# Optimization experiments

Measured on AMD Instinct MI355X. Metric: run time of the kernel, lower is better.

Reference implementation:

```python
import jax, jax.numpy as jnp
import numpy as np

N_NODES = 100000
N_EDGES = 800000
D_IN = 128
HOPS = 2
BN_EPS = 1e-5


def setup_inputs() -> dict:
    key = jax.random.key(0)
    ks = jax.random.split(key, 12)
    d_cat = D_IN * (HOPS + 1)  # 384
    inp = {
        "x": jax.random.normal(ks[0], (N_NODES, D_IN), dtype=jnp.float32),
        "edge_index": jax.random.randint(ks[1], (2, N_EDGES), 0, N_NODES, dtype=jnp.int32),
        "W0": jax.random.normal(ks[2], (HOPS + 1, D_IN, D_IN), dtype=jnp.float32) / np.sqrt(D_IN),
        "b0": jax.random.normal(ks[3], (HOPS + 1, D_IN), dtype=jnp.float32) * 0.01,
        "W1": jax.random.normal(ks[4], (HOPS + 1, d_cat, D_IN), dtype=jnp.float32) / np.sqrt(d_cat),
        "b1": jax.random.normal(ks[5], (HOPS + 1, D_IN), dtype=jnp.float32) * 0.01,
        "W2": jax.random.normal(ks[6], (HOPS + 1, d_cat, D_IN), dtype=jnp.float32) / np.sqrt(d_cat),
        "b2": jax.random.normal(ks[7], (HOPS + 1, D_IN), dtype=jnp.float32) * 0.01,
        "bn_gamma": jnp.ones((2, d_cat), dtype=jnp.float32),
        "bn_beta": jnp.zeros((2, d_cat), dtype=jnp.float32),
    }
    return inp


def _gcn_norm(edge_index, n):
    # gcn_norm(add_self_loops=False): deg over col, w_e = d^-1/2[row]*d^-1/2[col]
    row, col = edge_index[0], edge_index[1]
    deg = jax.ops.segment_sum(jnp.ones(row.shape[0], jnp.float32), col, num_segments=n)
    dinv = jnp.where(deg > 0, jax.lax.rsqrt(jnp.maximum(deg, 1.0)), 0.0)
    w = dinv[row] * dinv[col]
    return row, col, w


def _spmm(row, col, w, xj, n):
    # adj_t = SparseTensor(row=col, col=row, value=w): out[col_e] += w_e * x[row_e]
    return jax.ops.segment_sum(w[:, None] * xj[row], col, num_segments=n)


def _mixhop_layer(x, W, b, row, col, w, n):
    outs = [x @ W[0] + b[0]]
    for j in range(1, HOPS + 1):
        xj = x @ W[j] + b[j]
        for _ in range(j):
            xj = _spmm(row, col, w, xj, n)
        outs.append(xj)
    return jnp.concatenate(outs, axis=1)


def _bn(x, g, b):
    mu = jnp.mean(x, axis=0)
    var = jnp.mean(jnp.square(x - mu), axis=0)
    return (x - mu) * jax.lax.rsqrt(var + BN_EPS) * g + b


def reference(x, edge_index, W0, b0, W1, b1, W2, b2, bn_gamma, bn_beta):
    n = x.shape[0]
    row, col, w = _gcn_norm(edge_index, n)
    h = _mixhop_layer(x, W0, b0, row, col, w, n)
    h = jax.nn.relu(_bn(h, bn_gamma[0], bn_beta[0]))  # dropout: eval mode (identity)
    h = _mixhop_layer(h, W1, b1, row, col, w, n)
    h = jax.nn.relu(_bn(h, bn_gamma[1], bn_beta[1]))
    h = _mixhop_layer(h, W2, b2, row, col, w, n)
    return h
```

## Files before the change

### kernel.cpp

```cpp
#include <hip/hip_runtime.h>
#include <hip/hip_bf16.h>

#define NN 100000
#define NE 800000
#define DIN 128
#define DCAT 384
#define BN_EPS 1e-5

typedef __attribute__((ext_vector_type(8))) short bf16x8;
typedef __attribute__((ext_vector_type(4))) float f32x4;


__global__ void count_deg_k(const int* __restrict__ ei, int* __restrict__ deg) {
    int i = blockIdx.x * blockDim.x + threadIdx.x;
    if (i < NE) atomicAdd(&deg[ei[NE + i]], 1);
}

__global__ void dinv_k(const int* __restrict__ deg, float* __restrict__ dinv) {
    int i = blockIdx.x * blockDim.x + threadIdx.x;
    if (i < NN) {
        int d = deg[i];
        dinv[i] = (d > 0) ? rsqrtf((float)d) : 0.f;
    }
}

__global__ void scan1_k(const int* __restrict__ deg, int* __restrict__ out,
                        int* __restrict__ bsum) {
    __shared__ int s[1024];
    int i = blockIdx.x * 1024 + threadIdx.x;
    int v = (i < NN) ? deg[i] : 0;
    s[threadIdx.x] = v;
    __syncthreads();
    for (int off = 1; off < 1024; off <<= 1) {
        int t = (threadIdx.x >= off) ? s[threadIdx.x - off] : 0;
        __syncthreads();
        s[threadIdx.x] += t;
        __syncthreads();
    }
    if (i < NN) out[i] = s[threadIdx.x] - v;
    if (threadIdx.x == 1023) bsum[blockIdx.x] = s[1023];
}

__global__ void scan2_k(int* __restrict__ bsum, int nb) {
    if (threadIdx.x == 0) {
        int acc = 0;
        for (int b = 0; b < nb; ++b) { int v = bsum[b]; bsum[b] = acc; acc += v; }
    }
}

__global__ void scan3_k(int* __restrict__ ptr, int* __restrict__ cursor,
                        const int* __restrict__ bsum) {
    int i = blockIdx.x * 1024 + threadIdx.x;
    if (i < NN) {
        int p = ptr[i] + bsum[blockIdx.x];
        ptr[i] = p;
        cursor[i] = p;
    }
    if (i == NN) ptr[NN] = NE;
}

__global__ void scatter_k(const int* __restrict__ ei, const float* __restrict__ dinv,
                          int* __restrict__ cursor, int* __restrict__ crow,
                          float* __restrict__ cw) {
    int i = blockIdx.x * blockDim.x + threadIdx.x;
    if (i >= NE) return;
    int r = ei[i];
    int c = ei[NE + i];
    int p = atomicAdd(&cursor[c], 1);
    crow[p] = r;
    cw[p] = dinv[r] * dinv[c];
}


__device__ inline void split_trunc(float x, short& hi, short& lo) {
    unsigned u = __builtin_bit_cast(unsigned, x);
    hi = (short)(u >> 16);
    float hf = __builtin_bit_cast(float, u & 0xFFFF0000u);
    __hip_bfloat16 l = __float2bfloat16(x - hf);
    lo = *reinterpret_cast<short*>(&l);
}

__global__ void wsplit_k(const float* __restrict__ W, int K,
                         short* __restrict__ Wth, short* __restrict__ Wtl) {
    int i = blockIdx.x * 256 + threadIdx.x;
    if (i >= 3 * K * 128) return;
    int c = i & 127;
    int k = (i >> 7) % K;
    int j = i / (K * 128);
    short h, l;
    split_trunc(W[i], h, l);
    size_t o = (size_t)j * 128 * 384 + (size_t)c * 384 + k;
    Wth[o] = h;
    Wtl[o] = l;
}

#define GPITCH 40

__global__ __launch_bounds__(256, 2) void gemm3m_k(
    const float* __restrict__ X, int K,
    const short* __restrict__ Wth, const short* __restrict__ Wtl,
    const float* __restrict__ bias,
    const float2* __restrict__ coef, int use_bn,
    float* __restrict__ o0, float* __restrict__ o1, float* __restrict__ o2) {
    __shared__ short As_h[128 * GPITCH];
    __shared__ short As_l[128 * GPITCH];
    __shared__ short Bs_h[128 * GPITCH];
    __shared__ short Bs_l[128 * GPITCH];

    const int nwg = gridDim.x;
    const int id  = blockIdx.x;
    const int q = nwg >> 3, r = nwg & 7;
    const int xcd = id & 7, ii = id >> 3;
    const int swz = (xcd < r ? xcd * (q + 1) : r * (q + 1) + (xcd - r) * q) + ii;
    const int j  = swz % 3;
    const int my = swz / 3;
    const int m0 = my * 128;

    const int t    = threadIdx.x;
    const int lane = t & 63;
    const int wv   = t >> 6;
    const int wr   = (wv >> 1) * 64;
    const int wc   = (wv & 1) * 64;
    const int lr   = lane & 15;
    const int lk   = lane >> 4;

    const short* Wh = Wth + (size_t)j * 128 * 384;
    const short* Wl = Wtl + (size_t)j * 128 * 384;

    f32x4 acc[4][4];
#pragma unroll
    for (int a = 0; a < 4; ++a)
#pragma unroll
        for (int b = 0; b < 4; ++b) acc[a][b] = (f32x4){0.f, 0.f, 0.f, 0.f};

    for (int kb = 0; kb < K; kb += 32) {
#pragma unroll
        for (int i = 0; i < 4; ++i) {
            int lin = t + i * 256;
            int row = lin >> 3, kq = lin & 7;
            int gr = m0 + row;
            if (gr >= NN) gr = NN - 1;
            float4 a4 = *(const float4*)(X + (size_t)gr * K + kb + kq * 4);
            if (use_bn) {
                int c = kb + kq * 4;
                float2 c0 = coef[c + 0], c1 = coef[c + 1], c2 = coef[c + 2], c3 = coef[c + 3];
                a4.x = fmaxf(a4.x * c0.x + c0.y, 0.f);
                a4.y = fmaxf(a4.y * c1.x + c1.y, 0.f);
                a4.z = fmaxf(a4.z * c2.x + c2.y, 0.f);
                a4.w = fmaxf(a4.w * c3.x + c3.y, 0.f);
            }
            short h0, l0, h1, l1, h2, l2, h3, l3;
            split_trunc(a4.x, h0, l0);
            split_trunc(a4.y, h1, l1);
            split_trunc(a4.z, h2, l2);
            split_trunc(a4.w, h3, l3);
            *(short4*)&As_h[row * GPITCH + kq * 4] = make_short4(h0, h1, h2, h3);
            *(short4*)&As_l[row * GPITCH + kq * 4] = make_short4(l0, l1, l2, l3);
        }
#pragma unroll
        for (int i = 0; i < 4; ++i) {
            int lin = t + i * 256;
            int col = lin >> 3, kq = lin & 7;
            short4 bh = *(const short4*)(Wh + (size_t)col * 384 + kb + kq * 4);
            short4 bl = *(const short4*)(Wl + (size_t)col * 384 + kb + kq * 4);
            *(short4*)&Bs_h[col * GPITCH + kq * 4] = bh;
            *(short4*)&Bs_l[col * GPITCH + kq * 4] = bl;
        }
        __syncthreads();

        bf16x8 ah[4], al[4];
#pragma unroll
        for (int mr = 0; mr < 4; ++mr) {
            int rr = wr + mr * 16 + lr;
            ah[mr] = *(const bf16x8*)&As_h[rr * GPITCH + lk * 8];
            al[mr] = *(const bf16x8*)&As_l[rr * GPITCH + lk * 8];
        }
#pragma unroll
        for (int nc = 0; nc < 4; ++nc) {
            int c = wc + nc * 16 + lr;
            bf16x8 bh = *(const bf16x8*)&Bs_h[c * GPITCH + lk * 8];
            bf16x8 bl = *(const bf16x8*)&Bs_l[c * GPITCH + lk * 8];
#pragma unroll
            for (int mr = 0; mr < 4; ++mr) {
                f32x4 a = acc[mr][nc];
                a = __builtin_amdgcn_mfma_f32_16x16x32_bf16(al[mr], bh, a, 0, 0, 0);
                a = __builtin_amdgcn_mfma_f32_16x16x32_bf16(ah[mr], bl, a, 0, 0, 0);
                a = __builtin_amdgcn_mfma_f32_16x16x32_bf16(ah[mr], bh, a, 0, 0, 0);
                acc[mr][nc] = a;
            }
        }
        __syncthreads();
    }

    float* dst;
    int pitch;
    if (j == 0)      { dst = o0; pitch = DCAT; }
    else if (j == 1) { dst = o1; pitch = 128; }
    else             { dst = o2; pitch = 128; }

#pragma unroll
    for (int nc = 0; nc < 4; ++nc) {
        int col = wc + nc * 16 + lr;
        float bv = bias[j * 128 + col];
#pragma unroll
        for (int mr = 0; mr < 4; ++mr) {
            f32x4 a = acc[mr][nc];
#pragma unroll
            for (int rr = 0; rr < 4; ++rr) {
                int row = m0 + wr + mr * 16 + lk * 4 + rr;
                if (row < NN) dst[(size_t)row * pitch + col] = a[rr] + bv;
            }
        }
    }
}

__global__ __launch_bounds__(256) void spmm2_k(
    const int* __restrict__ ptr, const int* __restrict__ rows,
    const float* __restrict__ wv,
    const float* __restrict__ inA, const float* __restrict__ inB,
    float* __restrict__ outA, int poutA,
    float* __restrict__ outB) {
    int wid  = (blockIdx.x * blockDim.x + threadIdx.x) >> 6;
    int lane = threadIdx.x & 63;
    if (wid >= NN) return;
    int e0 = ptr[wid], e1 = ptr[wid + 1];
    float2 aA = make_float2(0.f, 0.f), aB = make_float2(0.f, 0.f);
    int e = e0;
    for (; e + 2 <= e1; e += 2) {
        int   r0 = rows[e],  r1 = rows[e + 1];
        float w0 = wv[e],    w1 = wv[e + 1];
        float2 vA0 = ((const float2*)(inA + (size_t)r0 * 128))[lane];
        float2 vB0 = ((const float2*)(inB + (size_t)r0 * 128))[lane];
        float2 vA1 = ((const float2*)(inA + (size_t)r1 * 128))[lane];
        float2 vB1 = ((const float2*)(inB + (size_t)r1 * 128))[lane];
        aA.x += w0 * vA0.x; aA.y += w0 * vA0.y;
        aB.x += w0 * vB0.x; aB.y += w0 * vB0.y;
        aA.x += w1 * vA1.x; aA.y += w1 * vA1.y;
        aB.x += w1 * vB1.x; aB.y += w1 * vB1.y;
    }
    if (e < e1) {
        int   r0 = rows[e];
        float w0 = wv[e];
        float2 vA0 = ((const float2*)(inA + (size_t)r0 * 128))[lane];
        float2 vB0 = ((const float2*)(inB + (size_t)r0 * 128))[lane];
        aA.x += w0 * vA0.x; aA.y += w0 * vA0.y;
        aB.x += w0 * vB0.x; aB.y += w0 * vB0.y;
    }
    ((float2*)(outA + (size_t)wid * poutA))[lane] = aA;
    ((float2*)(outB + (size_t)wid * 128))[lane] = aB;
}

__global__ __launch_bounds__(256) void spmm_k(
    const int* __restrict__ ptr, const int* __restrict__ rows,
    const float* __restrict__ wv, const float* __restrict__ xin, int pin,
    float* __restrict__ xout, int pout) {
    int wid  = (blockIdx.x * blockDim.x + threadIdx.x) >> 6;
    int lane = threadIdx.x & 63;
    if (wid >= NN) return;
    int e0 = ptr[wid], e1 = ptr[wid + 1];
    float2 acc = make_float2(0.f, 0.f);
    int e = e0;
    for (; e + 4 <= e1; e += 4) {
        int   r0 = rows[e],     r1 = rows[e + 1], r2 = rows[e + 2], r3 = rows[e + 3];
        float w0 = wv[e],       w1 = wv[e + 1],   w2 = wv[e + 2],   w3 = wv[e + 3];
        float2 v0 = ((const float2*)(xin + (size_t)r0 * pin))[lane];
        float2 v1 = ((const float2*)(xin + (size_t)r1 * pin))[lane];
        float2 v2 = ((const float2*)(xin + (size_t)r2 * pin))[lane];
        float2 v3 = ((const float2*)(xin + (size_t)r3 * pin))[lane];
        acc.x += w0 * v0.x; acc.y += w0 * v0.y;
        acc.x += w1 * v1.x; acc.y += w1 * v1.y;
        acc.x += w2 * v2.x; acc.y += w2 * v2.y;
        acc.x += w3 * v3.x; acc.y += w3 * v3.y;
    }
    for (; e < e1; ++e) {
        int   r0 = rows[e];
        float w0 = wv[e];
        float2 v0 = ((const float2*)(xin + (size_t)r0 * pin))[lane];
        acc.x += w0 * v0.x; acc.y += w0 * v0.y;
    }
    ((float2*)(xout + (size_t)wid * pout))[lane] = acc;
}

#define BN_ROWS 256
#define BN_NBLK ((NN + BN_ROWS - 1) / BN_ROWS)

__global__ void bn_stats1_k(const float* __restrict__ H, float* __restrict__ partial) {
    int c  = threadIdx.x;
    int r0 = blockIdx.x * BN_ROWS;
    int r1 = min(r0 + BN_ROWS, NN);
    float s = 0.f, s2 = 0.f;
    for (int r = r0; r < r1; ++r) {
        float v = H[(size_t)r * DCAT + c];
        s  += v;
        s2 += v * v;
    }
    partial[blockIdx.x * 768 + c]       = s;
    partial[blockIdx.x * 768 + 384 + c] = s2;
}

__global__ void bn_finalize_k(const float* __restrict__ partial,
                              const float* __restrict__ g, const float* __restrict__ b,
                              float2* __restrict__ coef) {
    int c = threadIdx.x;
    double s = 0.0, s2 = 0.0;
    for (int i = 0; i < BN_NBLK; ++i) {
        s  += (double)partial[i * 768 + c];
        s2 += (double)partial[i * 768 + 384 + c];
    }
    double mu  = s / (double)NN;
    double var = s2 / (double)NN - mu * mu;
    double inv = 1.0 / sqrt(var + (double)BN_EPS);
    float scale = (float)((double)g[c] * inv);
    float shift = (float)((double)b[c] - mu * (double)g[c] * inv);
    coef[c] = make_float2(scale, shift);
}


static void run_layer(const float* X, int K, const float* W, const float* bias,
                      const float2* coefIn, int use_bn,
                      float* Hout, float* tmpA, float* tmpB, float* tmpC,
                      short* Wth, short* Wtl,
                      const int* ptr, const int* crow, const float* cw,
                      hipStream_t stream) {
    int nw = 3 * K * 128;
    wsplit_k<<<(nw + 255) / 256, 256, 0, stream>>>(W, K, Wth, Wtl);
    int nwg = 3 * ((NN + 127) / 128);
    gemm3m_k<<<nwg, 256, 0, stream>>>(X, K, Wth, Wtl, bias, coefIn, use_bn,
                                      Hout, tmpA, tmpB);
    int sg = (NN * 64 + 255) / 256;
    spmm2_k<<<sg, 256, 0, stream>>>(ptr, crow, cw, tmpA, tmpB, Hout + 128, DCAT, tmpC);
    spmm_k<<<sg, 256, 0, stream>>>(ptr, crow, cw, tmpC, 128, Hout + 256, DCAT);
}

static void run_bn_stats(const float* H, const float* g, const float* b,
                         float* partial, float2* coef, hipStream_t stream) {
    bn_stats1_k<<<BN_NBLK, 384, 0, stream>>>(H, partial);
    bn_finalize_k<<<1, 384, 0, stream>>>(partial, g, b, coef);
}

extern "C" void kernel_launch(void* const* d_in, const int* in_sizes, int n_in,
                              void* d_out, int out_size, void* d_ws, size_t ws_size,
                              hipStream_t stream) {
    const float* x        = (const float*)d_in[0];
    const int*   ei       = (const int*)d_in[1];
    const float* W0       = (const float*)d_in[2];
    const float* b0       = (const float*)d_in[3];
    const float* W1       = (const float*)d_in[4];
    const float* b1       = (const float*)d_in[5];
    const float* W2       = (const float*)d_in[6];
    const float* b2       = (const float*)d_in[7];
    const float* bn_gamma = (const float*)d_in[8];
    const float* bn_beta  = (const float*)d_in[9];
    float* out = (float*)d_out;

    char* p = (char*)d_ws;
    auto alloc = [&](size_t bytes) -> void* {
        void* r = (void*)p;
        p += (bytes + 511) & ~(size_t)511;
        return r;
    };
    float* Hws     = (float*)alloc((size_t)NN * DCAT * 4);
    float* tmpA    = (float*)alloc((size_t)NN * 128 * 4);
    float* tmpB    = (float*)alloc((size_t)NN * 128 * 4);
    int*   deg     = (int*)alloc((size_t)NN * 4);
    float* dinv    = (float*)alloc((size_t)NN * 4);
    int*   ptr     = (int*)alloc((size_t)(NN + 1) * 4);
    int*   cursor  = (int*)alloc((size_t)NN * 4);
    int*   bsum    = (int*)alloc(1024);
    int*   crow    = (int*)alloc((size_t)NE * 4);
    float* cw      = (float*)alloc((size_t)NE * 4);
    float* partial = (float*)alloc((size_t)BN_NBLK * 768 * 4);
    float2* coef   = (float2*)alloc(384 * 8);
    short* Wth     = (short*)alloc((size_t)3 * 128 * 384 * 2);
    short* Wtl     = (short*)alloc((size_t)3 * 128 * 384 * 2);

    hipMemsetAsync(deg, 0, (size_t)NN * 4, stream);
    count_deg_k<<<(NE + 255) / 256, 256, 0, stream>>>(ei, deg);
    dinv_k<<<(NN + 255) / 256, 256, 0, stream>>>(deg, dinv);
    int nsb = (NN + 1023) / 1024;
    scan1_k<<<nsb, 1024, 0, stream>>>(deg, ptr, bsum);
    scan2_k<<<1, 64, 0, stream>>>(bsum, nsb);
    scan3_k<<<nsb, 1024, 0, stream>>>(ptr, cursor, bsum);
    scatter_k<<<(NE + 255) / 256, 256, 0, stream>>>(ei, dinv, cursor, crow, cw);

    run_layer(x, DIN, W0, b0, coef, 0, out, tmpA, tmpB, Hws,
              Wth, Wtl, ptr, crow, cw, stream);
    run_bn_stats(out, bn_gamma, bn_beta, partial, coef, stream);

    run_layer(out, DCAT, W1, b1, coef, 1, Hws, tmpA, tmpB, out,
              Wth, Wtl, ptr, crow, cw, stream);
    run_bn_stats(Hws, bn_gamma + DCAT, bn_beta + DCAT, partial, coef, stream);

    run_layer(Hws, DCAT, W2, b2, coef, 1, out, tmpA, tmpB, Hws,
              Wth, Wtl, ptr, crow, cw, stream);
}
```

Baseline: 1.702 ms.

## Presplit activations to bf16 hi/lo, double-buffer GEMM A tile, widen SpMM gathers

A new bnsplit_k pass applies the BatchNorm+ReLU affine and splits activations into bf16 high/low planes once, so the GEMM no longer repeats that split for each of the three weight slices. The GEMM now double-buffers only the A tile in LDS and reads B fragments straight from global memory into registers, with occupancy raised to 3 waves per SIMD. The two hop intermediates are interleaved into a single 256-wide buffer, so spmm2 does one float4 gather per edge. spmm_k splits each wavefront into two half-waves that handle alternate edges with float4 loads and combine via a shuffle. The trade-off is an extra full read/write pass per layer, plus tmpC reusing the Xh buffer.

```diff
diff --git a/kernel.cpp b/kernel.cpp
--- a/kernel.cpp
+++ b/kernel.cpp
@@ -9,6 +9,7 @@
 
 typedef __attribute__((ext_vector_type(8))) short bf16x8;
 typedef __attribute__((ext_vector_type(4))) float f32x4;
+typedef __attribute__((ext_vector_type(4))) int   i32x4;
 
 
 __global__ void count_deg_k(const int* __restrict__ ei, int* __restrict__ deg) {
@@ -94,18 +95,44 @@
     Wtl[o] = l;
 }
 
+__global__ __launch_bounds__(256) void bnsplit_k(
+    const float* __restrict__ H, int Kc4,
+    const float2* __restrict__ coef, int use_bn,
+    short* __restrict__ Xh, short* __restrict__ Xl) {
+    size_t n4 = (size_t)NN * Kc4;
+    for (size_t i = (size_t)blockIdx.x * blockDim.x + threadIdx.x; i < n4;
+         i += (size_t)gridDim.x * blockDim.x) {
+        float4 v = ((const float4*)H)[i];
+        if (use_bn) {
+            int c4 = (int)(i % Kc4) * 4;
+            float2 c0 = coef[c4 + 0], c1 = coef[c4 + 1];
+            float2 c2 = coef[c4 + 2], c3 = coef[c4 + 3];
+            v.x = fmaxf(v.x * c0.x + c0.y, 0.f);
+            v.y = fmaxf(v.y * c1.x + c1.y, 0.f);
+            v.z = fmaxf(v.z * c2.x + c2.y, 0.f);
+            v.w = fmaxf(v.w * c3.x + c3.y, 0.f);
+        }
+        short h0, l0, h1, l1, h2, l2, h3, l3;
+        split_trunc(v.x, h0, l0);
+        split_trunc(v.y, h1, l1);
+        split_trunc(v.z, h2, l2);
+        split_trunc(v.w, h3, l3);
+        ((short4*)Xh)[i] = make_short4(h0, h1, h2, h3);
+        ((short4*)Xl)[i] = make_short4(l0, l1, l2, l3);
+    }
+}
+
 #define GPITCH 40
 
-__global__ __launch_bounds__(256, 2) void gemm3m_k(
-    const float* __restrict__ X, int K,
+__global__ __launch_bounds__(256, 3) void gemm3m_k(
+    const short* __restrict__ Xh, const short* __restrict__ Xl, int K,
     const short* __restrict__ Wth, const short* __restrict__ Wtl,
     const float* __restrict__ bias,
-    const float2* __restrict__ coef, int use_bn,
-    float* __restrict__ o0, float* __restrict__ o1, float* __restrict__ o2) {
-    __shared__ short As_h[128 * GPITCH];
-    __shared__ short As_l[128 * GPITCH];
-    __shared__ short Bs_h[128 * GPITCH];
-    __shared__ short Bs_l[128 * GPITCH];
+    float* __restrict__ o0, int p0,
+    float* __restrict__ o1, int p1,
+    float* __restrict__ o2, int p2) {
+    __shared__ short Ah[2][128 * GPITCH];
+    __shared__ short Al[2][128 * GPITCH];
 
     const int nwg = gridDim.x;
     const int id  = blockIdx.x;
@@ -113,8 +140,7 @@
     const int xcd = id & 7, ii = id >> 3;
     const int swz = (xcd < r ? xcd * (q + 1) : r * (q + 1) + (xcd - r) * q) + ii;
     const int j  = swz % 3;
-    const int my = swz / 3;
-    const int m0 = my * 128;
+    const int m0 = (swz / 3) * 128;
 
     const int t    = threadIdx.x;
     const int lane = t & 63;
@@ -127,76 +153,91 @@
     const short* Wh = Wth + (size_t)j * 128 * 384;
     const short* Wl = Wtl + (size_t)j * 128 * 384;
 
+    const int arow = t >> 1;
+    const int akc  = (t & 1) * 16;
+    int gr = m0 + arow;
+    if (gr >= NN) gr = NN - 1;
+    const short* pAh = Xh + (size_t)gr * K + akc;
+    const short* pAl = Xl + (size_t)gr * K + akc;
+    const int soff = arow * GPITCH + akc;
+
     f32x4 acc[4][4];
 #pragma unroll
     for (int a = 0; a < 4; ++a)
 #pragma unroll
         for (int b = 0; b < 4; ++b) acc[a][b] = (f32x4){0.f, 0.f, 0.f, 0.f};
 
-    for (int kb = 0; kb < K; kb += 32) {
-#pragma unroll
-        for (int i = 0; i < 4; ++i) {
-            int lin = t + i * 256;
-            int row = lin >> 3, kq = lin & 7;
-            int gr = m0 + row;
-            if (gr >= NN) gr = NN - 1;
-            float4 a4 = *(const float4*)(X + (size_t)gr * K + kb + kq * 4);
-            if (use_bn) {
-                int c = kb + kq * 4;
-                float2 c0 = coef[c + 0], c1 = coef[c + 1], c2 = coef[c + 2], c3 = coef[c + 3];
-                a4.x = fmaxf(a4.x * c0.x + c0.y, 0.f);
-                a4.y = fmaxf(a4.y * c1.x + c1.y, 0.f);
-                a4.z = fmaxf(a4.z * c2.x + c2.y, 0.f);
-                a4.w = fmaxf(a4.w * c3.x + c3.y, 0.f);
-            }
-            short h0, l0, h1, l1, h2, l2, h3, l3;
-            split_trunc(a4.x, h0, l0);
-            split_trunc(a4.y, h1, l1);
-            split_trunc(a4.z, h2, l2);
-            split_trunc(a4.w, h3, l3);
-            *(short4*)&As_h[row * GPITCH + kq * 4] = make_short4(h0, h1, h2, h3);
-            *(short4*)&As_l[row * GPITCH + kq * 4] = make_short4(l0, l1, l2, l3);
-        }
-#pragma unroll
-        for (int i = 0; i < 4; ++i) {
-            int lin = t + i * 256;
-            int col = lin >> 3, kq = lin & 7;
-            short4 bh = *(const short4*)(Wh + (size_t)col * 384 + kb + kq * 4);
-            short4 bl = *(const short4*)(Wl + (size_t)col * 384 + kb + kq * 4);
-            *(short4*)&Bs_h[col * GPITCH + kq * 4] = bh;
-            *(short4*)&Bs_l[col * GPITCH + kq * 4] = bl;
-        }
-        __syncthreads();
+    const int NT = K >> 5;
+
+    {
+        i32x4 h0 = *(const i32x4*)(pAh);
+        i32x4 h1 = *(const i32x4*)(pAh + 8);
+        i32x4 l0 = *(const i32x4*)(pAl);
+        i32x4 l1 = *(const i32x4*)(pAl + 8);
+        *(i32x4*)&Ah[0][soff]     = h0;
+        *(i32x4*)&Ah[0][soff + 8] = h1;
+        *(i32x4*)&Al[0][soff]     = l0;
+        *(i32x4*)&Al[0][soff + 8] = l1;
+    }
+    __syncthreads();
+
+    int cur = 0;
+    for (int tt = 0; tt < NT; ++tt) {
+        const int kb = tt << 5;
+
+        bf16x8 bh[4], bl[4];
+#pragma unroll
+        for (int nc = 0; nc < 4; ++nc) {
+            const size_t bo = (size_t)(wc + nc * 16 + lr) * 384 + kb + lk * 8;
+            bh[nc] = *(const bf16x8*)(Wh + bo);
+            bl[nc] = *(const bf16x8*)(Wl + bo);
+        }
+
+        i32x4 h0, h1, l0, l1;
+        if (tt + 1 < NT) {
+            const int ko = kb + 32;
+            h0 = *(const i32x4*)(pAh + ko);
+            h1 = *(const i32x4*)(pAh + ko + 8);
+            l0 = *(const i32x4*)(pAl + ko);
+            l1 = *(const i32x4*)(pAl + ko + 8);
+        }
 
         bf16x8 ah[4], al[4];
 #pragma unroll
         for (int mr = 0; mr < 4; ++mr) {
-            int rr = wr + mr * 16 + lr;
-            ah[mr] = *(const bf16x8*)&As_h[rr * GPITCH + lk * 8];
-            al[mr] = *(const bf16x8*)&As_l[rr * GPITCH + lk * 8];
-        }
+            const int rr = (wr + mr * 16 + lr) * GPITCH + lk * 8;
+            ah[mr] = *(const bf16x8*)&Ah[cur][rr];
+            al[mr] = *(const bf16x8*)&Al[cur][rr];
+        }
+
 #pragma unroll
         for (int nc = 0; nc < 4; ++nc) {
-            int c = wc + nc * 16 + lr;
-            bf16x8 bh = *(const bf16x8*)&Bs_h[c * GPITCH + lk * 8];
-            bf16x8 bl = *(const bf16x8*)&Bs_l[c * GPITCH + lk * 8];
 #pragma unroll
             for (int mr = 0; mr < 4; ++mr) {
                 f32x4 a = acc[mr][nc];
-                a = __builtin_amdgcn_mfma_f32_16x16x32_bf16(al[mr], bh, a, 0, 0, 0);
-                a = __builtin_amdgcn_mfma_f32_16x16x32_bf16(ah[mr], bl, a, 0, 0, 0);
-                a = __builtin_amdgcn_mfma_f32_16x16x32_bf16(ah[mr], bh, a, 0, 0, 0);
+                a = __builtin_amdgcn_mfma_f32_16x16x32_bf16(al[mr], bh[nc], a, 0, 0, 0);
+                a = __builtin_amdgcn_mfma_f32_16x16x32_bf16(ah[mr], bl[nc], a, 0, 0, 0);
+                a = __builtin_amdgcn_mfma_f32_16x16x32_bf16(ah[mr], bh[nc], a, 0, 0, 0);
                 acc[mr][nc] = a;
             }
         }
+
+        if (tt + 1 < NT) {
+            const int nb = cur ^ 1;
+            *(i32x4*)&Ah[nb][soff]     = h0;
+            *(i32x4*)&Ah[nb][soff + 8] = h1;
+            *(i32x4*)&Al[nb][soff]     = l0;
+            *(i32x4*)&Al[nb][soff + 8] = l1;
+        }
         __syncthreads();
+        cur ^= 1;
     }
 
     float* dst;
     int pitch;
-    if (j == 0)      { dst = o0; pitch = DCAT; }
-    else if (j == 1) { dst = o1; pitch = 128; }
-    else             { dst = o2; pitch = 128; }
+    if (j == 0)      { dst = o0; pitch = p0; }
+    else if (j == 1) { dst = o1; pitch = p1; }
+    else             { dst = o2; pitch = p2; }
 
 #pragma unroll
     for (int nc = 0; nc < 4; ++nc) {
@@ -217,68 +258,85 @@
 __global__ __launch_bounds__(256) void spmm2_k(
     const int* __restrict__ ptr, const int* __restrict__ rows,
     const float* __restrict__ wv,
-    const float* __restrict__ inA, const float* __restrict__ inB,
-    float* __restrict__ outA, int poutA,
+    const float* __restrict__ inAB,
+    float* __restrict__ outA,
     float* __restrict__ outB) {
     int wid  = (blockIdx.x * blockDim.x + threadIdx.x) >> 6;
     int lane = threadIdx.x & 63;
     if (wid >= NN) return;
     int e0 = ptr[wid], e1 = ptr[wid + 1];
-    float2 aA = make_float2(0.f, 0.f), aB = make_float2(0.f, 0.f);
+    float4 acc = make_float4(0.f, 0.f, 0.f, 0.f);
     int e = e0;
     for (; e + 2 <= e1; e += 2) {
         int   r0 = rows[e],  r1 = rows[e + 1];
         float w0 = wv[e],    w1 = wv[e + 1];
-        float2 vA0 = ((const float2*)(inA + (size_t)r0 * 128))[lane];
-        float2 vB0 = ((const float2*)(inB + (size_t)r0 * 128))[lane];
-        float2 vA1 = ((const float2*)(inA + (size_t)r1 * 128))[lane];
-        float2 vB1 = ((const float2*)(inB + (size_t)r1 * 128))[lane];
-        aA.x += w0 * vA0.x; aA.y += w0 * vA0.y;
-        aB.x += w0 * vB0.x; aB.y += w0 * vB0.y;
-        aA.x += w1 * vA1.x; aA.y += w1 * vA1.y;
-        aB.x += w1 * vB1.x; aB.y += w1 * vB1.y;
+        float4 v0 = ((const float4*)(inAB + (size_t)r0 * 256))[lane];
+        float4 v1 = ((const float4*)(inAB + (size_t)r1 * 256))[lane];
+        acc.x += w0 * v0.x + w1 * v1.x;
+        acc.y += w0 * v0.y + w1 * v1.y;
+        acc.z += w0 * v0.z + w1 * v1.z;
+        acc.w += w0 * v0.w + w1 * v1.w;
     }
     if (e < e1) {
         int   r0 = rows[e];
         float w0 = wv[e];
-        float2 vA0 = ((const float2*)(inA + (size_t)r0 * 128))[lane];
-        float2 vB0 = ((const float2*)(inB + (size_t)r0 * 128))[lane];
-        aA.x += w0 * vA0.x; aA.y += w0 * vA0.y;
-        aB.x += w0 * vB0.x; aB.y += w0 * vB0.y;
-    }
-    ((float2*)(outA + (size_t)wid * poutA))[lane] = aA;
-    ((float2*)(outB + (size_t)wid * 128))[lane] = aB;
+        float4 v0 = ((const float4*)(inAB + (size_t)r0 * 256))[lane];
+        acc.x += w0 * v0.x;
+        acc.y += w0 * v0.y;
+        acc.z += w0 * v0.z;
+        acc.w += w0 * v0.w;
+    }
+    if (lane < 32) ((float4*)(outA + (size_t)wid * 384))[lane] = acc;
+    else           ((float4*)(outB + (size_t)wid * 128))[lane - 32] = acc;
 }
 
 __global__ __launch_bounds__(256) void spmm_k(
     const int* __restrict__ ptr, const int* __restrict__ rows,
-    const float* __restrict__ wv, const float* __restrict__ xin, int pin,
+    const float* __restrict__ wv,
+    const float* __restrict__ xin,
     float* __restrict__ xout, int pout) {
     int wid  = (blockIdx.x * blockDim.x + threadIdx.x) >> 6;
     int lane = threadIdx.x & 63;
     if (wid >= NN) return;
     int e0 = ptr[wid], e1 = ptr[wid + 1];
-    float2 acc = make_float2(0.f, 0.f);
+    int half = lane >> 5;
+    int cl   = lane & 31;
+    float4 acc = make_float4(0.f, 0.f, 0.f, 0.f);
     int e = e0;
     for (; e + 4 <= e1; e += 4) {
-        int   r0 = rows[e],     r1 = rows[e + 1], r2 = rows[e + 2], r3 = rows[e + 3];
-        float w0 = wv[e],       w1 = wv[e + 1],   w2 = wv[e + 2],   w3 = wv[e + 3];
-        float2 v0 = ((const float2*)(xin + (size_t)r0 * pin))[lane];
-        float2 v1 = ((const float2*)(xin + (size_t)r1 * pin))[lane];
-        float2 v2 = ((const float2*)(xin + (size_t)r2 * pin))[lane];
-        float2 v3 = ((const float2*)(xin + (size_t)r3 * pin))[lane];
-        acc.x += w0 * v0.x; acc.y += w0 * v0.y;
-        acc.x += w1 * v1.x; acc.y += w1 * v1.y;
-        acc.x += w2 * v2.x; acc.y += w2 * v2.y;
-        acc.x += w3 * v3.x; acc.y += w3 * v3.y;
-    }
-    for (; e < e1; ++e) {
-        int   r0 = rows[e];
-        float w0 = wv[e];
-        float2 v0 = ((const float2*)(xin + (size_t)r0 * pin))[lane];
-        acc.x += w0 * v0.x; acc.y += w0 * v0.y;
-    }
-    ((float2*)(xout + (size_t)wid * pout))[lane] = acc;
+        int   ra = rows[e + half],     rb = rows[e + 2 + half];
+        float wa = wv[e + half],       wb = wv[e + 2 + half];
+        float4 va = ((const float4*)(xin + (size_t)ra * 128))[cl];
+        float4 vb = ((const float4*)(xin + (size_t)rb * 128))[cl];
+        acc.x += wa * va.x + wb * vb.x;
+        acc.y += wa * va.y + wb * vb.y;
+        acc.z += wa * va.z + wb * vb.z;
+        acc.w += wa * va.w + wb * vb.w;
+    }
+    for (; e + 2 <= e1; e += 2) {
+        int   ra = rows[e + half];
+        float wa = wv[e + half];
+        float4 va = ((const float4*)(xin + (size_t)ra * 128))[cl];
+        acc.x += wa * va.x;
+        acc.y += wa * va.y;
+        acc.z += wa * va.z;
+        acc.w += wa * va.w;
+    }
+    if (e < e1 && half == 0) {
+        int   ra = rows[e];
+        float wa = wv[e];
+        float4 va = ((const float4*)(xin + (size_t)ra * 128))[cl];
+        acc.x += wa * va.x;
+        acc.y += wa * va.y;
+        acc.z += wa * va.z;
+        acc.w += wa * va.w;
+    }
+    float4 o;
+    o.x = acc.x + __shfl_xor(acc.x, 32);
+    o.y = acc.y + __shfl_xor(acc.y, 32);
+    o.z = acc.z + __shfl_xor(acc.z, 32);
+    o.w = acc.w + __shfl_xor(acc.w, 32);
+    if (half == 0) ((float4*)(xout + (size_t)wid * pout))[cl] = o;
 }
 
 #define BN_ROWS 256
@@ -316,26 +374,20 @@
 }
 
 
-static void run_layer(const float* X, int K, const float* W, const float* bias,
-                      const float2* coefIn, int use_bn,
-                      float* Hout, float* tmpA, float* tmpB, float* tmpC,
+static void run_layer(const short* Xh, const short* Xl, int K,
+                      const float* W, const float* bias,
+                      float* Hout, float* tmpAB, float* tmpC,
                       short* Wth, short* Wtl,
                       const int* ptr, const int* crow, const float* cw,
                       hipStream_t stream) {
     int nw = 3 * K * 128;
     wsplit_k<<<(nw + 255) / 256, 256, 0, stream>>>(W, K, Wth, Wtl);
     int nwg = 3 * ((NN + 127) / 128);
-    gemm3m_k<<<nwg, 256, 0, stream>>>(X, K, Wth, Wtl, bias, coefIn, use_bn,
-                                      Hout, tmpA, tmpB);
+    gemm3m_k<<<nwg, 256, 0, stream>>>(Xh, Xl, K, Wth, Wtl, bias,
+                                      Hout, DCAT, tmpAB, 256, tmpAB + 128, 256);
     int sg = (NN * 64 + 255) / 256;
-    spmm2_k<<<sg, 256, 0, stream>>>(ptr, crow, cw, tmpA, tmpB, Hout + 128, DCAT, tmpC);
-    spmm_k<<<sg, 256, 0, stream>>>(ptr, crow, cw, tmpC, 128, Hout + 256, DCAT);
-}
-
-static void run_bn_stats(const float* H, const float* g, const float* b,
-                         float* partial, float2* coef, hipStream_t stream) {
-    bn_stats1_k<<<BN_NBLK, 384, 0, stream>>>(H, partial);
-    bn_finalize_k<<<1, 384, 0, stream>>>(partial, g, b, coef);
+    spmm2_k<<<sg, 256, 0, stream>>>(ptr, crow, cw, tmpAB, Hout + 128, tmpC);
+    spmm_k<<<sg, 256, 0, stream>>>(ptr, crow, cw, tmpC, Hout + 256, DCAT);
 }
 
 extern "C" void kernel_launch(void* const* d_in, const int* in_sizes, int n_in,
@@ -359,9 +411,10 @@
         p += (bytes + 511) & ~(size_t)511;
         return r;
     };
+    short* Xh      = (short*)alloc((size_t)NN * DCAT * 2);
+    short* Xl      = (short*)alloc((size_t)NN * DCAT * 2);
+    float* tmpAB   = (float*)alloc((size_t)NN * 256 * 4);
     float* Hws     = (float*)alloc((size_t)NN * DCAT * 4);
-    float* tmpA    = (float*)alloc((size_t)NN * 128 * 4);
-    float* tmpB    = (float*)alloc((size_t)NN * 128 * 4);
     int*   deg     = (int*)alloc((size_t)NN * 4);
     float* dinv    = (float*)alloc((size_t)NN * 4);
     int*   ptr     = (int*)alloc((size_t)(NN + 1) * 4);
@@ -373,6 +426,7 @@
     float2* coef   = (float2*)alloc(384 * 8);
     short* Wth     = (short*)alloc((size_t)3 * 128 * 384 * 2);
     short* Wtl     = (short*)alloc((size_t)3 * 128 * 384 * 2);
+    float* tmpC = (float*)Xh;
 
     hipMemsetAsync(deg, 0, (size_t)NN * 4, stream);
     count_deg_k<<<(NE + 255) / 256, 256, 0, stream>>>(ei, deg);
@@ -383,14 +437,16 @@
     scan3_k<<<nsb, 1024, 0, stream>>>(ptr, cursor, bsum);
     scatter_k<<<(NE + 255) / 256, 256, 0, stream>>>(ei, dinv, cursor, crow, cw);
 
-    run_layer(x, DIN, W0, b0, coef, 0, out, tmpA, tmpB, Hws,
-              Wth, Wtl, ptr, crow, cw, stream);
-    run_bn_stats(out, bn_gamma, bn_beta, partial, coef, stream);
-
-    run_layer(out, DCAT, W1, b1, coef, 1, Hws, tmpA, tmpB, out,
-              Wth, Wtl, ptr, crow, cw, stream);
-    run_bn_stats(Hws, bn_gamma + DCAT, bn_beta + DCAT, partial, coef, stream);
-
-    run_layer(Hws, DCAT, W2, b2, coef, 1, out, tmpA, tmpB, Hws,
-              Wth, Wtl, ptr, crow, cw, stream);
-}
+    bnsplit_k<<<2048, 256, 0, stream>>>(x, DIN / 4, coef, 0, Xh, Xl);
+    run_layer(Xh, Xl, DIN, W0, b0, out, tmpAB, tmpC, Wth, Wtl, ptr, crow, cw, stream);
+    bn_stats1_k<<<BN_NBLK, 384, 0, stream>>>(out, partial);
+    bn_finalize_k<<<1, 384, 0, stream>>>(partial, bn_gamma, bn_beta, coef);
+
+    bnsplit_k<<<2048, 256, 0, stream>>>(out, DCAT / 4, coef, 1, Xh, Xl);
+    run_layer(Xh, Xl, DCAT, W1, b1, Hws, tmpAB, tmpC, Wth, Wtl, ptr, crow, cw, stream);
+    bn_stats1_k<<<BN_NBLK, 384, 0, stream>>>(Hws, partial);
+    bn_finalize_k<<<1, 384, 0, stream>>>(partial, bn_gamma + DCAT, bn_beta + DCAT, coef);
+
+    bnsplit_k<<<2048, 256, 0, stream>>>(Hws, DCAT / 4, coef, 1, Xh, Xl);
+    run_layer(Xh, Xl, DCAT, W2, b2, out, tmpAB, tmpC, Wth, Wtl, ptr, crow, cw, stream);
+}
```

Result: slower. 1.813 ms (+6.5%).
